# Kernel tuning notes

Hardware: AMD Instinct MI355X
Metric: run time of the kernel (lower is better)

The kernel has to match this reference:

```python
import jax, jax.numpy as jnp
import numpy as np

B, P, ENC = 64, 196, 2048          # batch, num_pixels (14x14), encoder_dim
A, E, D, V = 512, 512, 512, 20000  # attention_dim, embed_dim, decoder_dim, vocab
MAXLEN = 22
T = MAXLEN - 1                     # decode steps (teacher forcing drops last token)


def _lin(k, fan_in, fan_out, scale=0.02):
    return jax.random.normal(k, (fan_in, fan_out), jnp.float32) * scale, jnp.zeros((fan_out,), jnp.float32)


def setup_inputs() -> dict:
    key = jax.random.key(0)
    ks = jax.random.split(key, 16)
    encoder_out = jax.random.normal(ks[0], (B, P, ENC), jnp.float32)
    captions = jax.random.randint(ks[1], (B, MAXLEN), 0, V)
    lens = jax.random.randint(ks[2], (B,), 2, MAXLEN + 1)
    lens = jnp.sort(lens)[::-1].at[0].set(MAXLEN)  # sorted descending, as the torch loop assumes
    emb = jax.random.uniform(ks[3], (V, E), jnp.float32, -0.1, 0.1)
    enc_att_w, enc_att_b = _lin(ks[4], ENC, A)
    dec_att_w, dec_att_b = _lin(ks[5], D, A)
    full_att_w, full_att_b = _lin(ks[6], A, 1)
    w_ih = jax.random.normal(ks[7], (E + ENC, 4 * D), jnp.float32) * 0.02
    w_hh = jax.random.normal(ks[8], (D, 4 * D), jnp.float32) * 0.02
    b_ih = jnp.zeros((4 * D,), jnp.float32)
    b_hh = jnp.zeros((4 * D,), jnp.float32)
    init_h_w, init_h_b = _lin(ks[9], ENC, D)
    init_c_w, init_c_b = _lin(ks[10], ENC, D)
    f_beta_w, f_beta_b = _lin(ks[11], D, ENC)
    fc_w = jax.random.uniform(ks[12], (D, V), jnp.float32, -0.1, 0.1)
    fc_b = jnp.zeros((V,), jnp.float32)
    return dict(encoder_out=encoder_out, captions=captions, lengths=lens, emb=emb,
                enc_att_w=enc_att_w, enc_att_b=enc_att_b, dec_att_w=dec_att_w, dec_att_b=dec_att_b,
                full_att_w=full_att_w, full_att_b=full_att_b, w_ih=w_ih, b_ih=b_ih, w_hh=w_hh, b_hh=b_hh,
                init_h_w=init_h_w, init_h_b=init_h_b, init_c_w=init_c_w, init_c_b=init_c_b,
                f_beta_w=f_beta_w, f_beta_b=f_beta_b, fc_w=fc_w, fc_b=fc_b)


def reference(encoder_out, captions, lengths, emb,
              enc_att_w, enc_att_b, dec_att_w, dec_att_b, full_att_w, full_att_b,
              w_ih, b_ih, w_hh, b_hh, init_h_w, init_h_b, init_c_w, init_c_b,
              f_beta_w, f_beta_b, fc_w, fc_b):
    # Dropout is identity (eval mode) for a deterministic reference.
    dec_len = lengths - 1                       # decode_lengths
    x_emb = emb[captions]                       # (B, L, E)
    mean_enc = encoder_out.mean(axis=1)         # (B, ENC)
    h0 = mean_enc @ init_h_w + init_h_b         # (B, D)
    c0 = mean_enc @ init_c_w + init_c_b
    att1 = encoder_out @ enc_att_w + enc_att_b  # (B, P, A), hoisted out of the loop

    emb_ts = jnp.swapaxes(x_emb[:, :T, :], 0, 1)  # (T, B, E)
    t_idx = jnp.arange(T)

    def step(carry, xt):
        h, c = carry
        e_t, t = xt
        active = (t < dec_len)[:, None]         # ragged batch -> mask (sorted lengths)
        # Bahdanau attention
        att2 = h @ dec_att_w + dec_att_b        # (B, A)
        scores = (jax.nn.relu(att1 + att2[:, None, :]) @ full_att_w)[..., 0] + full_att_b[0]  # (B, P)
        alpha = jax.nn.softmax(scores, axis=1)
        context = jnp.einsum('bp,bpe->be', alpha, encoder_out)
        # gated context
        gate = jax.nn.sigmoid(h @ f_beta_w + f_beta_b)
        context = gate * context
        # LSTMCell (torch gate order i, f, g, o)
        x = jnp.concatenate([e_t, context], axis=1)
        gates = x @ w_ih + h @ w_hh + b_ih + b_hh
        i_g, f_g, g_g, o_g = jnp.split(gates, 4, axis=1)
        c_new = jax.nn.sigmoid(f_g) * c + jax.nn.sigmoid(i_g) * jnp.tanh(g_g)
        h_new = jax.nn.sigmoid(o_g) * jnp.tanh(c_new)
        h = jnp.where(active, h_new, h)
        c = jnp.where(active, c_new, c)
        preds = jnp.where(active, h_new @ fc_w + fc_b, 0.0)
        alpha_o = jnp.where(active, alpha, 0.0)
        return (h, c), (preds, alpha_o)

    _, (preds, alphas) = jax.lax.scan(step, (h0, c0), (emb_ts, t_idx))
    predictions = jnp.swapaxes(preds, 0, 1)     # (B, T, V)
    alphas = jnp.swapaxes(alphas, 0, 1)         # (B, T, P)
    return predictions, alphas
```

## Files before the change

### kernel.cpp

```cpp
#include <hip/hip_runtime.h>

#define BB   64
#define PP   196
#define ENC  2048
#define AA   512
#define EE   512
#define DD   512
#define VV   20000
#define TT   21
#define ML   22

#define PRED_ELEMS ((size_t)BB * TT * VV)

typedef __attribute__((ext_vector_type(8))) short s8bf;
typedef __attribute__((ext_vector_type(4))) float f4acc;

__device__ __forceinline__ float bf2f(unsigned short u) {
    union { unsigned int i; float f; } v; v.i = ((unsigned int)u) << 16; return v.f;
}
__device__ __forceinline__ void unpack2(unsigned int u, float& lo, float& hi) {
    union { unsigned int i; float f; } a, b;
    a.i = u << 16; b.i = u & 0xFFFF0000u; lo = a.f; hi = b.f;
}
__device__ __forceinline__ unsigned short f2bf(float f) {
    union { float f; unsigned int i; } v; v.f = f;
    unsigned int i = v.i;
    return (unsigned short)((i + 0x7FFFu + ((i >> 16) & 1u)) >> 16);
}
__device__ __forceinline__ float sigmoidf(float x) { return 1.0f / (1.0f + __expf(-x)); }

template <bool F> __device__ __forceinline__ float ldw(const void* p, size_t i) {
    if (F) return ((const float*)p)[i];
    return bf2f(((const unsigned short*)p)[i]);
}
template <bool F> __device__ __forceinline__ unsigned short ldbf(const void* p, size_t i) {
    if (F) return f2bf(((const float*)p)[i]);
    return ((const unsigned short*)p)[i];
}
template <bool F> __device__ __forceinline__ float2 ld2(const void* p, size_t i) {
    if (F) return *(const float2*)((const float*)p + i);
    unsigned int u = *(const unsigned int*)((const unsigned short*)p + i);
    float lo, hi; unpack2(u, lo, hi); return make_float2(lo, hi);
}
template <bool F> __device__ __forceinline__ float4 ld4(const void* p, size_t i) {
    if (F) return *(const float4*)((const float*)p + i);
    uint2 u = *(const uint2*)((const unsigned short*)p + i);
    float a, b, c, d; unpack2(u.x, a, b); unpack2(u.y, c, d);
    return make_float4(a, b, c, d);
}
template <bool F> __device__ __forceinline__ void st1(void* p, size_t i, float v) {
    if (F) ((float*)p)[i] = v; else ((unsigned short*)p)[i] = f2bf(v);
}

__global__ void dec_detect_kernel(const unsigned short* __restrict__ enc_us, int* __restrict__ flag) {
    __shared__ int s_cnt;
    if (threadIdx.x == 0) s_cnt = 0;
    __syncthreads();
    int cnt = 0;
    for (int i = threadIdx.x; i < 8192; i += 256) {
        unsigned short u = enc_us[2 * i];
        if ((u & 0x7F80) == 0x7F80) cnt++;
    }
    if (cnt) atomicAdd(&s_cnt, cnt);
    __syncthreads();
    if (threadIdx.x == 0) *flag = (s_cnt > 0) ? 1 : 0;
}

template <bool F>
__device__ __forceinline__ void conv_swz_body(const void* W, int K, int Norig,
                                              unsigned short* dst, int permMode, int nChunks) {
    int chunk = blockIdx.x * 4 + (threadIdx.x >> 6);
    if (chunk >= nChunks) return;
    int lane = threadIdx.x & 63;
    int KC = K >> 5;
    int nt = chunk / KC, kc = chunk % KC;
    int quad = lane >> 4, l15 = lane & 15;
    int np = nt * 16 + l15;
    int col;
    if (permMode == 1) col = ((np >> 4) & 3) * 512 + (np >> 6) * 16 + (np & 15);
    else col = np;
    union { s8bf v; unsigned short s[8]; } o;
    if (np < Norig || permMode == 1) {
        size_t base = (size_t)(kc * 32 + quad * 8) * Norig + col;
#pragma unroll
        for (int j = 0; j < 8; ++j) o.s[j] = ldbf<F>(W, base + (size_t)j * Norig);
    } else {
#pragma unroll
        for (int j = 0; j < 8; ++j) o.s[j] = 0;
    }
    *(s8bf*)(dst + ((size_t)chunk * 64 + lane) * 8) = o.v;
}
__global__ void conv_swz_kernel(const int* __restrict__ flg, const void* __restrict__ W,
                                int K, int Norig, unsigned short* __restrict__ dst,
                                int permMode, int nChunks) {
    if (*flg) conv_swz_body<true>(W, K, Norig, dst, permMode, nChunks);
    else      conv_swz_body<false>(W, K, Norig, dst, permMode, nChunks);
}

template <bool F>
__device__ __forceinline__ void conv_bias_body(const void* dab, const void* fbb,
                                               const void* bih, const void* bhh, const void* fcb,
                                               const void* ihb, const void* icb, const void* eab,
                                               float* ag_b, float* g_b, float* fc_b,
                                               float* ihb_f, float* icb_f, float* eab_f) {
    int i = blockIdx.x * 256 + threadIdx.x;
    if (i < 2560) ag_b[i] = (i < 512) ? ldw<F>(dab, i) : ldw<F>(fbb, i - 512);
    else if (i < 2560 + 2048) {
        int np = i - 2560;
        int orig = ((np >> 4) & 3) * 512 + (np >> 6) * 16 + (np & 15);
        g_b[np] = ldw<F>(bih, orig) + ldw<F>(bhh, orig);
    } else if (i < 2560 + 2048 + 20000) fc_b[i - 4608] = ldw<F>(fcb, i - 4608);
    else if (i < 2560 + 2048 + 20000 + 512) ihb_f[i - 24608] = ldw<F>(ihb, i - 24608);
    else if (i < 2560 + 2048 + 20000 + 1024) icb_f[i - 25120] = ldw<F>(icb, i - 25120);
    else if (i < 2560 + 2048 + 20000 + 1536) eab_f[i - 25632] = ldw<F>(eab, i - 25632);
}
__global__ void conv_bias_kernel(const int* __restrict__ flg,
                                 const void* dab, const void* fbb, const void* bih, const void* bhh,
                                 const void* fcb, const void* ihb, const void* icb, const void* eab,
                                 float* ag_b, float* g_b, float* fc_b,
                                 float* ihb_f, float* icb_f, float* eab_f) {
    if (*flg) conv_bias_body<true>(dab, fbb, bih, bhh, fcb, ihb, icb, eab, ag_b, g_b, fc_b, ihb_f, icb_f, eab_f);
    else      conv_bias_body<false>(dab, fbb, bih, bhh, fcb, ihb, icb, eab, ag_b, g_b, fc_b, ihb_f, icb_f, eab_f);
}

template <bool F>
__device__ __forceinline__ void mean_body(const void* enc, unsigned short* mean_bf) {
    int b = blockIdx.x;
    int e = blockIdx.y * 256 + threadIdx.x;
    size_t base = (size_t)b * PP * ENC + e;
    float s = 0.f;
#pragma unroll 4
    for (int p = 0; p < PP; ++p) s += ldw<F>(enc, base + (size_t)p * ENC);
    mean_bf[b * ENC + e] = f2bf(s * (1.0f / (float)PP));
}
__global__ void dec_mean_kernel(const void* __restrict__ enc, const int* __restrict__ flg,
                                unsigned short* __restrict__ mean_bf) {
    if (*flg) mean_body<true>(enc, mean_bf); else mean_body<false>(enc, mean_bf);
}

__global__ __launch_bounds__(256)
void gemm_u_kernel(const int* __restrict__ flg,
                   const unsigned short* __restrict__ A1, int K1, const unsigned short* __restrict__ W1,
                   const unsigned short* __restrict__ A2, int K2, const unsigned short* __restrict__ W2,
                   const float* __restrict__ bias, int N, int epi, int nct,
                   float* __restrict__ outF, float* __restrict__ outF2,
                   unsigned short* __restrict__ hb, float* __restrict__ cptr,
                   unsigned short* __restrict__ h_all,
                   void* __restrict__ outV, const int* __restrict__ lengths, int t) {
    __shared__ float s_g[4 * 64 * 17];
    int tid = threadIdx.x;
    int wave = tid >> 6, lane = tid & 63;
    int l15 = lane & 15, quad = lane >> 4;
    const unsigned short* Abase1 = A1;
    if (epi == 2) Abase1 = A1 + (size_t)blockIdx.x * 64 * K1;
    f4acc acc[4][2];
#pragma unroll
    for (int a = 0; a < 4; ++a) { acc[a][0] = (f4acc)0.f; acc[a][1] = (f4acc)0.f; }
#pragma unroll
    for (int pass = 0; pass < 2; ++pass) {
        const unsigned short* A = pass ? A2 : Abase1;
        if (!A) continue;
        int K = pass ? K2 : K1;
        const unsigned short* W = pass ? W2 : W1;
        int KC = K >> 5;
        for (int kc = 0; kc < KC; ++kc) {
            s8bf af[4];
#pragma unroll
            for (int rt = 0; rt < 4; ++rt)
                af[rt] = *(const s8bf*)(A + (size_t)(rt * 16 + l15) * K + kc * 32 + quad * 8);
#pragma unroll
            for (int ct = 0; ct < 2; ++ct) if (ct < nct) {
                int nt = blockIdx.y * 4 * nct + ct * 4 + wave;
                s8bf bv = *(const s8bf*)(W + ((size_t)(nt * KC + kc) * 64 + lane) * 8);
#pragma unroll
                for (int rt = 0; rt < 4; ++rt)
                    acc[rt][ct] = __builtin_amdgcn_mfma_f32_16x16x32_bf16(af[rt], bv, acc[rt][ct], 0, 0, 0);
            }
        }
    }
    if (epi == 4) {
        int nl = wave * 16 + l15;
        int g = (nl >> 4) & 3, dl = nl & 15;
        float bv = bias[blockIdx.y * 64 + nl];
#pragma unroll
        for (int rt = 0; rt < 4; ++rt)
#pragma unroll
            for (int r = 0; r < 4; ++r) {
                int m = rt * 16 + quad * 4 + r;
                s_g[(g * 64 + m) * 17 + dl] = acc[rt][0][r] + bv;
            }
        __syncthreads();
        int m = tid >> 2;
        bool act = t < (lengths[m] - 1);
#pragma unroll
        for (int i = 0; i < 4; ++i) {
            int dl2 = (tid & 3) * 4 + i;
            int d = blockIdx.y * 16 + dl2;
            unsigned short hv;
            if (act) {
                float ig = sigmoidf(s_g[(0 * 64 + m) * 17 + dl2]);
                float fg = sigmoidf(s_g[(1 * 64 + m) * 17 + dl2]);
                float gg = tanhf(s_g[(2 * 64 + m) * 17 + dl2]);
                float og = sigmoidf(s_g[(3 * 64 + m) * 17 + dl2]);
                float cn = fg * cptr[m * DD + d] + ig * gg;
                float hn = og * tanhf(cn);
                cptr[m * DD + d] = cn;
                hv = f2bf(hn);
            } else {
                hv = A2[(size_t)m * K2 + d];
            }
            hb[m * DD + d] = hv;
            h_all[((size_t)t * BB + m) * DD + d] = hv;
        }
        return;
    }
    bool f32o = (epi == 2) ? (*flg != 0) : false;
    int tb = blockIdx.x;
#pragma unroll
    for (int ct = 0; ct < 2; ++ct) if (ct < nct) {
        int n = blockIdx.y * 64 * nct + ct * 64 + wave * 16 + l15;
        if (n >= N) continue;
        float bv = bias ? bias[n] : 0.f;
#pragma unroll
        for (int rt = 0; rt < 4; ++rt)
#pragma unroll
            for (int r = 0; r < 4; ++r) {
                int m = rt * 16 + quad * 4 + r;
                float v = acc[rt][ct][r] + bv;
                if (epi == 0)      outF[(size_t)m * N + n] = v;
                else if (epi == 1) {
                    if (n < 512) outF[(size_t)m * 512 + n] = v;
                    else         outF2[(size_t)m * 2048 + (n - 512)] = sigmoidf(v);
                } else if (epi == 3) hb[(size_t)m * DD + n] = f2bf(v);
                else {
                    bool act = tb < (lengths[m] - 1);
                    float pv = act ? v : 0.f;
                    size_t oi = ((size_t)m * TT + tb) * VV + n;
                    if (f32o) ((float*)outV)[oi] = pv; else ((unsigned short*)outV)[oi] = f2bf(pv);
                }
            }
    }
}

template <bool F>
__device__ __forceinline__ void att1_gemm_body(const void* enc, const unsigned short* Wsw,
                                               const float* bias, float* att1) {
    __shared__ __attribute__((aligned(16))) unsigned short As[64 * 40];
    int tid = threadIdx.x;
    int wave = tid >> 6, lane = tid & 63;
    int l15 = lane & 15, quad = lane >> 4;
    int row0 = blockIdx.x * 64;
    f4acc acc[4][2];
#pragma unroll
    for (int a = 0; a < 4; ++a) { acc[a][0] = (f4acc)0.f; acc[a][1] = (f4acc)0.f; }
    int lr = tid >> 2, lk = (tid & 3) * 8;
    for (int kc = 0; kc < 64; ++kc) {
        int k0 = kc * 32;
        if (F) {
            const float* src = (const float*)enc + (size_t)(row0 + lr) * ENC + k0 + lk;
            float4 v0 = *(const float4*)src, v1 = *(const float4*)(src + 4);
            union { s8bf v; unsigned short s[8]; } t8;
            t8.s[0]=f2bf(v0.x); t8.s[1]=f2bf(v0.y); t8.s[2]=f2bf(v0.z); t8.s[3]=f2bf(v0.w);
            t8.s[4]=f2bf(v1.x); t8.s[5]=f2bf(v1.y); t8.s[6]=f2bf(v1.z); t8.s[7]=f2bf(v1.w);
            *(s8bf*)&As[lr * 40 + lk] = t8.v;
        } else {
            *(s8bf*)&As[lr * 40 + lk] =
                *(const s8bf*)((const unsigned short*)enc + (size_t)(row0 + lr) * ENC + k0 + lk);
        }
        __syncthreads();
        s8bf af[4];
#pragma unroll
        for (int rt = 0; rt < 4; ++rt)
            af[rt] = *(const s8bf*)&As[(rt * 16 + l15) * 40 + quad * 8];
#pragma unroll
        for (int ct = 0; ct < 2; ++ct) {
            int nt = blockIdx.y * 8 + ct * 4 + wave;
            s8bf bv = *(const s8bf*)(Wsw + ((size_t)(nt * 64 + kc) * 64 + lane) * 8);
#pragma unroll
            for (int rt = 0; rt < 4; ++rt)
                acc[rt][ct] = __builtin_amdgcn_mfma_f32_16x16x32_bf16(af[rt], bv, acc[rt][ct], 0, 0, 0);
        }
        __syncthreads();
    }
#pragma unroll
    for (int ct = 0; ct < 2; ++ct) {
        int n = blockIdx.y * 128 + ct * 64 + wave * 16 + l15;
        float bv = bias[n];
#pragma unroll
        for (int rt = 0; rt < 4; ++rt)
#pragma unroll
            for (int r = 0; r < 4; ++r) {
                int m = row0 + rt * 16 + quad * 4 + r;
                att1[(size_t)m * AA + n] = acc[rt][ct][r] + bv;
            }
    }
}
__global__ __launch_bounds__(256)
void gemm_att1_kernel(const void* __restrict__ enc, const int* __restrict__ flg,
                      const unsigned short* __restrict__ Wsw, const float* __restrict__ bias,
                      float* __restrict__ att1) {
    if (*flg) att1_gemm_body<true>(enc, Wsw, bias, att1);
    else      att1_gemm_body<false>(enc, Wsw, bias, att1);
}

template <bool F>
__device__ __forceinline__ void att_body(const float* att1, const float* att2,
                                         const void* faw, const void* fab,
                                         const int* lengths, float* alpha_ws, void* out, int t) {
    __shared__ float s_sc[256];
    __shared__ float s_red[256];
    int b = blockIdx.x, tid = threadIdx.x;
    int wave = tid >> 6, lane = tid & 63;
    int a0i = lane * 8;
    float4 a2a = *(const float4*)(att2 + (size_t)b * AA + a0i);
    float4 a2b = *(const float4*)(att2 + (size_t)b * AA + a0i + 4);
    float4 w0 = ld4<F>(faw, a0i);
    float4 w1 = ld4<F>(faw, a0i + 4);
    float fabv = ldw<F>(fab, 0);
    s_sc[tid] = -1e30f;
    __syncthreads();
#pragma unroll 2
    for (int r = wave; r < PP; r += 4) {
        const float4* row = (const float4*)(att1 + ((size_t)b * PP + r) * AA);
        float4 v0 = row[lane * 2];
        float4 v1 = row[lane * 2 + 1];
        float acc = fmaxf(v0.x + a2a.x, 0.f) * w0.x
                  + fmaxf(v0.y + a2a.y, 0.f) * w0.y
                  + fmaxf(v0.z + a2a.z, 0.f) * w0.z
                  + fmaxf(v0.w + a2a.w, 0.f) * w0.w
                  + fmaxf(v1.x + a2b.x, 0.f) * w1.x
                  + fmaxf(v1.y + a2b.y, 0.f) * w1.y
                  + fmaxf(v1.z + a2b.z, 0.f) * w1.z
                  + fmaxf(v1.w + a2b.w, 0.f) * w1.w;
#pragma unroll
        for (int off = 32; off; off >>= 1) acc += __shfl_xor(acc, off, 64);
        if (lane == 0) s_sc[r] = acc + fabv;
    }
    __syncthreads();
    float sc = s_sc[tid];
    s_red[tid] = sc;
    __syncthreads();
    for (int s = 128; s > 0; s >>= 1) { if (tid < s) s_red[tid] = fmaxf(s_red[tid], s_red[tid + s]); __syncthreads(); }
    float m = s_red[0];
    __syncthreads();
    float e = 0.f;
    if (tid < PP) e = __expf(sc - m);
    s_red[tid] = e;
    __syncthreads();
    for (int s = 128; s > 0; s >>= 1) { if (tid < s) s_red[tid] += s_red[tid + s]; __syncthreads(); }
    float inv = 1.0f / s_red[0];
    if (tid < PP) {
        float al = e * inv;
        alpha_ws[b * PP + tid] = al;
        bool active = t < (lengths[b] - 1);
        st1<F>(out, PRED_ELEMS + (size_t)(b * TT + t) * PP + tid, active ? al : 0.f);
    }
}
__global__ void dec_att_kernel(const float* __restrict__ att1, const float* __restrict__ att2,
                               const int* __restrict__ flg,
                               const void* __restrict__ faw, const void* __restrict__ fab,
                               const int* __restrict__ lengths,
                               float* __restrict__ alpha_ws, void* __restrict__ out, int t) {
    if (*flg) att_body<true>(att1, att2, faw, fab, lengths, alpha_ws, out, t);
    else      att_body<false>(att1, att2, faw, fab, lengths, alpha_ws, out, t);
}

template <bool F>
__device__ __forceinline__ void ctx_body(const void* enc, const float* alpha_ws, const float* gate,
                                         const void* emb, const int* captions,
                                         unsigned short* x_bf, int t) {
    __shared__ float s_al[PP];
    int b = blockIdx.x, yc = blockIdx.y, tid = threadIdx.x;
    if (tid < PP) s_al[tid] = alpha_ws[b * PP + tid];
    __syncthreads();
    if (yc == 0) {
        int cap = captions[b * ML + t];
        int i = tid * 2;
        float2 ev = ld2<F>(emb, (size_t)cap * EE + i);
        *(unsigned int*)(x_bf + (size_t)b * 2560 + i) =
            (unsigned int)f2bf(ev.x) | ((unsigned int)f2bf(ev.y) << 16);
    }
    int e = yc * 512 + tid * 2;
    float a0 = 0.f, a1 = 0.f;
    size_t base = (size_t)b * PP * ENC + e;
#pragma unroll 4
    for (int p = 0; p < PP; ++p) {
        float al = s_al[p];
        float2 v = ld2<F>(enc, base + (size_t)p * ENC);
        a0 += al * v.x; a1 += al * v.y;
    }
    float2 g = *(const float2*)&gate[(size_t)b * ENC + e];
    *(unsigned int*)(x_bf + (size_t)b * 2560 + EE + e) =
        (unsigned int)f2bf(a0 * g.x) | ((unsigned int)f2bf(a1 * g.y) << 16);
}
__global__ void dec_ctx_kernel(const void* __restrict__ enc, const int* __restrict__ flg,
                               const float* __restrict__ alpha_ws, const float* __restrict__ gate,
                               const void* __restrict__ emb, const int* __restrict__ captions,
                               unsigned short* __restrict__ x_bf, int t) {
    if (*flg) ctx_body<true>(enc, alpha_ws, gate, emb, captions, x_bf, t);
    else      ctx_body<false>(enc, alpha_ws, gate, emb, captions, x_bf, t);
}

extern "C" void kernel_launch(void* const* d_in, const int* in_sizes, int n_in,
                              void* d_out, int out_size, void* d_ws, size_t ws_size,
                              hipStream_t stream) {
    const void* enc      = d_in[0];
    const int* captions  = (const int*)d_in[1];
    const int* lengths   = (const int*)d_in[2];
    const void* emb      = d_in[3];
    const void* eaw      = d_in[4];
    const void* eab      = d_in[5];
    const void* daw      = d_in[6];
    const void* dab      = d_in[7];
    const void* faw      = d_in[8];
    const void* fab      = d_in[9];
    const void* wih      = d_in[10];
    const void* bih      = d_in[11];
    const void* whh      = d_in[12];
    const void* bhh      = d_in[13];
    const void* ihw      = d_in[14];
    const void* ihb      = d_in[15];
    const void* icw      = d_in[16];
    const void* icb      = d_in[17];
    const void* fbw      = d_in[18];
    const void* fbb      = d_in[19];
    const void* fcw      = d_in[20];
    const void* fcb      = d_in[21];

    char* cur = (char*)d_ws;
    auto alloc = [&](size_t bytes) { void* p = cur; cur += (bytes + 255) & ~(size_t)255; return p; };
    int* flg               = (int*)alloc(4);
    unsigned short* h_bufA = (unsigned short*)alloc((size_t)BB * DD * 2);
    unsigned short* h_bufB = (unsigned short*)alloc((size_t)BB * DD * 2);
    unsigned short* h_all  = (unsigned short*)alloc((size_t)TT * BB * DD * 2);
    unsigned short* x_bf   = (unsigned short*)alloc((size_t)BB * 2560 * 2);
    unsigned short* mean_bf= (unsigned short*)alloc((size_t)BB * ENC * 2);
    float* c               = (float*)alloc((size_t)BB * DD * 4);
    float* att2            = (float*)alloc((size_t)BB * AA * 4);
    float* gate            = (float*)alloc((size_t)BB * ENC * 4);
    float* alpha           = (float*)alloc((size_t)BB * PP * 4);
    float* ag_bias         = (float*)alloc(2560 * 4);
    float* g_bias          = (float*)alloc(2048 * 4);
    float* fc_bias         = (float*)alloc(20000 * 4);
    float* ihb_f           = (float*)alloc(512 * 4);
    float* icb_f           = (float*)alloc(512 * 4);
    float* eab_f           = (float*)alloc(512 * 4);
    unsigned short* eaw_sw = (unsigned short*)alloc((size_t)32 * 64 * 512 * 2);
    unsigned short* ag_sw  = (unsigned short*)alloc((size_t)160 * 16 * 512 * 2);
    unsigned short* ihw_sw = (unsigned short*)alloc((size_t)32 * 64 * 512 * 2);
    unsigned short* icw_sw = (unsigned short*)alloc((size_t)32 * 64 * 512 * 2);
    unsigned short* wih_sw = (unsigned short*)alloc((size_t)128 * 80 * 512 * 2);
    unsigned short* whh_sw = (unsigned short*)alloc((size_t)128 * 16 * 512 * 2);
    unsigned short* fcw_sw = (unsigned short*)alloc((size_t)1256 * 16 * 512 * 2);
    float* att1            = (float*)alloc((size_t)BB * PP * AA * 4);

    dec_detect_kernel<<<1, 256, 0, stream>>>((const unsigned short*)enc, flg);
    conv_swz_kernel<<<(32 * 64 + 3) / 4, 256, 0, stream>>>(flg, eaw, ENC, AA, eaw_sw, 0, 32 * 64);
    conv_swz_kernel<<<(32 * 16 + 3) / 4, 256, 0, stream>>>(flg, daw, DD, AA, ag_sw, 0, 32 * 16);
    conv_swz_kernel<<<(128 * 16 + 3) / 4, 256, 0, stream>>>(flg, fbw, DD, ENC, ag_sw + (size_t)32 * 16 * 512, 0, 128 * 16);
    conv_swz_kernel<<<(32 * 64 + 3) / 4, 256, 0, stream>>>(flg, ihw, ENC, DD, ihw_sw, 0, 32 * 64);
    conv_swz_kernel<<<(32 * 64 + 3) / 4, 256, 0, stream>>>(flg, icw, ENC, DD, icw_sw, 0, 32 * 64);
    conv_swz_kernel<<<(128 * 80 + 3) / 4, 256, 0, stream>>>(flg, wih, 2560, 2048, wih_sw, 1, 128 * 80);
    conv_swz_kernel<<<(128 * 16 + 3) / 4, 256, 0, stream>>>(flg, whh, DD, 2048, whh_sw, 1, 128 * 16);
    conv_swz_kernel<<<(1256 * 16 + 3) / 4, 256, 0, stream>>>(flg, fcw, DD, VV, fcw_sw, 0, 1256 * 16);
    conv_bias_kernel<<<(26144 + 255) / 256, 256, 0, stream>>>(flg, dab, fbb, bih, bhh, fcb, ihb, icb, eab,
                                                              ag_bias, g_bias, fc_bias, ihb_f, icb_f, eab_f);
    dec_mean_kernel<<<dim3(BB, ENC / 256), 256, 0, stream>>>(enc, flg, mean_bf);
    gemm_u_kernel<<<dim3(1, 4), 256, 0, stream>>>(flg, mean_bf, ENC, ihw_sw, nullptr, 0, nullptr,
                                                  ihb_f, DD, 3, 2, nullptr, nullptr, h_bufA, nullptr,
                                                  nullptr, nullptr, nullptr, 0);
    gemm_u_kernel<<<dim3(1, 4), 256, 0, stream>>>(flg, mean_bf, ENC, icw_sw, nullptr, 0, nullptr,
                                                  icb_f, DD, 0, 2, c, nullptr, nullptr, nullptr,
                                                  nullptr, nullptr, nullptr, 0);
    gemm_att1_kernel<<<dim3(196, 4), 256, 0, stream>>>(enc, flg, eaw_sw, eab_f, att1);

    unsigned short* hcur = h_bufA;
    for (int t = 0; t < TT; ++t) {
        unsigned short* hnext = (hcur == h_bufA) ? h_bufB : h_bufA;
        gemm_u_kernel<<<dim3(1, 40), 256, 0, stream>>>(flg, hcur, DD, ag_sw, nullptr, 0, nullptr,
                                                       ag_bias, 2560, 1, 1, att2, gate, nullptr, nullptr,
                                                       nullptr, nullptr, nullptr, 0);
        dec_att_kernel<<<BB, 256, 0, stream>>>(att1, att2, flg, faw, fab, lengths, alpha, d_out, t);
        dec_ctx_kernel<<<dim3(BB, 4), 256, 0, stream>>>(enc, flg, alpha, gate, emb, captions, x_bf, t);
        gemm_u_kernel<<<dim3(1, 32), 256, 0, stream>>>(flg, x_bf, 2560, wih_sw, hcur, DD, whh_sw,
                                                       g_bias, 2048, 4, 1, nullptr, nullptr, hnext, c,
                                                       h_all, nullptr, lengths, t);
        hcur = hnext;
    }
    gemm_u_kernel<<<dim3(TT, 157), 256, 0, stream>>>(flg, h_all, DD, fcw_sw, nullptr, 0, nullptr,
                                                     fc_bias, VV, 2, 2, nullptr, nullptr, nullptr, nullptr,
                                                     nullptr, d_out, lengths, 0);
}
```

Measured before the change: 3.098 ms.

## Store att1 and encoder copy in bf16, widen attention blocks, stage FC output through LDS

att1 is now stored as bf16 instead of fp32, and the attention kernel runs 1024 threads per batch row so each of its 16 waves scores a subset of pixels. When workspace allows, a one-time kernel converts encoder_out to bf16 so the per-step context reduction reads half the bytes. The final vocabulary GEMM epilogue now goes through shared memory and writes vectorized float4/packed bf16 rows instead of strided scalar stores. This halves per-step memory traffic on att1 and the encoder but adds bf16 rounding error to attention scores and context, plus one extra conversion pass and more workspace.

```diff
diff --git a/kernel.cpp b/kernel.cpp
--- a/kernel.cpp
+++ b/kernel.cpp
@@ -64,6 +64,25 @@
     if (cnt) atomicAdd(&s_cnt, cnt);
     __syncthreads();
     if (threadIdx.x == 0) *flag = (s_cnt > 0) ? 1 : 0;
+}
+
+template <bool F>
+__device__ __forceinline__ void encconv_body(const void* enc, unsigned short* dst) {
+    size_t i = ((size_t)blockIdx.x * 256 + threadIdx.x) * 8;
+    if (F) {
+        const float* s = (const float*)enc + i;
+        float4 v0 = *(const float4*)s, v1 = *(const float4*)(s + 4);
+        union { uint4 u; unsigned short h[8]; } o;
+        o.h[0]=f2bf(v0.x); o.h[1]=f2bf(v0.y); o.h[2]=f2bf(v0.z); o.h[3]=f2bf(v0.w);
+        o.h[4]=f2bf(v1.x); o.h[5]=f2bf(v1.y); o.h[6]=f2bf(v1.z); o.h[7]=f2bf(v1.w);
+        *(uint4*)(dst + i) = o.u;
+    } else {
+        *(uint4*)(dst + i) = *(const uint4*)((const unsigned short*)enc + i);
+    }
+}
+__global__ void enc_bf_kernel(const void* __restrict__ enc, const int* __restrict__ flg,
+                              unsigned short* __restrict__ dst) {
+    if (*flg) encconv_body<true>(enc, dst); else encconv_body<false>(enc, dst);
 }
 
 template <bool F>
@@ -147,7 +166,7 @@
                    unsigned short* __restrict__ hb, float* __restrict__ cptr,
                    unsigned short* __restrict__ h_all,
                    void* __restrict__ outV, const int* __restrict__ lengths, int t) {
-    __shared__ float s_g[4 * 64 * 17];
+    __shared__ float s_g[64 * 132];
     int tid = threadIdx.x;
     int wave = tid >> 6, lane = tid & 63;
     int l15 = lane & 15, quad = lane >> 4;
@@ -214,8 +233,46 @@
         }
         return;
     }
-    bool f32o = (epi == 2) ? (*flg != 0) : false;
-    int tb = blockIdx.x;
+    if (epi == 2) {
+        int t2 = blockIdx.x;
+        int base_n = blockIdx.y * 128;
+#pragma unroll
+        for (int ct = 0; ct < 2; ++ct) {
+            int nl = ct * 64 + wave * 16 + l15;
+            int nn = base_n + nl;
+            float bv = (nn < VV) ? bias[nn] : 0.f;
+#pragma unroll
+            for (int rt = 0; rt < 4; ++rt)
+#pragma unroll
+                for (int r = 0; r < 4; ++r) {
+                    int m = rt * 16 + quad * 4 + r;
+                    s_g[m * 132 + nl] = acc[rt][ct][r] + bv;
+                }
+        }
+        __syncthreads();
+        bool f32o = (*flg != 0);
+#pragma unroll
+        for (int pass = 0; pass < 8; ++pass) {
+            int m = pass * 8 + (tid >> 5);
+            int j = tid & 31;
+            int n = base_n + j * 4;
+            if (n < VV) {
+                bool act = t2 < (lengths[m] - 1);
+                float4 v = *(const float4*)&s_g[m * 132 + j * 4];
+                if (!act) { v.x = 0.f; v.y = 0.f; v.z = 0.f; v.w = 0.f; }
+                size_t oi = ((size_t)m * TT + t2) * VV + n;
+                if (f32o) {
+                    *(float4*)((float*)outV + oi) = v;
+                } else {
+                    uint2 pk;
+                    pk.x = (unsigned int)f2bf(v.x) | ((unsigned int)f2bf(v.y) << 16);
+                    pk.y = (unsigned int)f2bf(v.z) | ((unsigned int)f2bf(v.w) << 16);
+                    *(uint2*)((unsigned short*)outV + oi) = pk;
+                }
+            }
+        }
+        return;
+    }
 #pragma unroll
     for (int ct = 0; ct < 2; ++ct) if (ct < nct) {
         int n = blockIdx.y * 64 * nct + ct * 64 + wave * 16 + l15;
@@ -232,19 +289,13 @@
                     if (n < 512) outF[(size_t)m * 512 + n] = v;
                     else         outF2[(size_t)m * 2048 + (n - 512)] = sigmoidf(v);
                 } else if (epi == 3) hb[(size_t)m * DD + n] = f2bf(v);
-                else {
-                    bool act = tb < (lengths[m] - 1);
-                    float pv = act ? v : 0.f;
-                    size_t oi = ((size_t)m * TT + tb) * VV + n;
-                    if (f32o) ((float*)outV)[oi] = pv; else ((unsigned short*)outV)[oi] = f2bf(pv);
-                }
             }
     }
 }
 
 template <bool F>
 __device__ __forceinline__ void att1_gemm_body(const void* enc, const unsigned short* Wsw,
-                                               const float* bias, float* att1) {
+                                               const float* bias, unsigned short* att1) {
     __shared__ __attribute__((aligned(16))) unsigned short As[64 * 40];
     int tid = threadIdx.x;
     int wave = tid >> 6, lane = tid & 63;
@@ -291,20 +342,20 @@
 #pragma unroll
             for (int r = 0; r < 4; ++r) {
                 int m = row0 + rt * 16 + quad * 4 + r;
-                att1[(size_t)m * AA + n] = acc[rt][ct][r] + bv;
+                att1[(size_t)m * AA + n] = f2bf(acc[rt][ct][r] + bv);
             }
     }
 }
 __global__ __launch_bounds__(256)
 void gemm_att1_kernel(const void* __restrict__ enc, const int* __restrict__ flg,
                       const unsigned short* __restrict__ Wsw, const float* __restrict__ bias,
-                      float* __restrict__ att1) {
+                      unsigned short* __restrict__ att1) {
     if (*flg) att1_gemm_body<true>(enc, Wsw, bias, att1);
     else      att1_gemm_body<false>(enc, Wsw, bias, att1);
 }
 
 template <bool F>
-__device__ __forceinline__ void att_body(const float* att1, const float* att2,
+__device__ __forceinline__ void att_body(const unsigned short* att1, const float* att2,
                                          const void* faw, const void* fab,
                                          const int* lengths, float* alpha_ws, void* out, int t) {
     __shared__ float s_sc[256];
@@ -317,35 +368,35 @@
     float4 w0 = ld4<F>(faw, a0i);
     float4 w1 = ld4<F>(faw, a0i + 4);
     float fabv = ldw<F>(fab, 0);
-    s_sc[tid] = -1e30f;
-    __syncthreads();
-#pragma unroll 2
-    for (int r = wave; r < PP; r += 4) {
-        const float4* row = (const float4*)(att1 + ((size_t)b * PP + r) * AA);
-        float4 v0 = row[lane * 2];
-        float4 v1 = row[lane * 2 + 1];
-        float acc = fmaxf(v0.x + a2a.x, 0.f) * w0.x
-                  + fmaxf(v0.y + a2a.y, 0.f) * w0.y
-                  + fmaxf(v0.z + a2a.z, 0.f) * w0.z
-                  + fmaxf(v0.w + a2a.w, 0.f) * w0.w
-                  + fmaxf(v1.x + a2b.x, 0.f) * w1.x
-                  + fmaxf(v1.y + a2b.y, 0.f) * w1.y
-                  + fmaxf(v1.z + a2b.z, 0.f) * w1.z
-                  + fmaxf(v1.w + a2b.w, 0.f) * w1.w;
+    if (tid < 256) s_sc[tid] = -1e30f;
+    __syncthreads();
+    for (int r = wave; r < PP; r += 16) {
+        uint4 u = *(const uint4*)(att1 + ((size_t)b * PP + r) * AA + a0i);
+        float v0, v1, v2, v3, v4, v5, v6, v7;
+        unpack2(u.x, v0, v1); unpack2(u.y, v2, v3);
+        unpack2(u.z, v4, v5); unpack2(u.w, v6, v7);
+        float acc = fmaxf(v0 + a2a.x, 0.f) * w0.x
+                  + fmaxf(v1 + a2a.y, 0.f) * w0.y
+                  + fmaxf(v2 + a2a.z, 0.f) * w0.z
+                  + fmaxf(v3 + a2a.w, 0.f) * w0.w
+                  + fmaxf(v4 + a2b.x, 0.f) * w1.x
+                  + fmaxf(v5 + a2b.y, 0.f) * w1.y
+                  + fmaxf(v6 + a2b.z, 0.f) * w1.z
+                  + fmaxf(v7 + a2b.w, 0.f) * w1.w;
 #pragma unroll
         for (int off = 32; off; off >>= 1) acc += __shfl_xor(acc, off, 64);
         if (lane == 0) s_sc[r] = acc + fabv;
     }
     __syncthreads();
-    float sc = s_sc[tid];
-    s_red[tid] = sc;
+    float sc = (tid < 256) ? s_sc[tid] : -1e30f;
+    if (tid < 256) s_red[tid] = sc;
     __syncthreads();
     for (int s = 128; s > 0; s >>= 1) { if (tid < s) s_red[tid] = fmaxf(s_red[tid], s_red[tid + s]); __syncthreads(); }
     float m = s_red[0];
     __syncthreads();
     float e = 0.f;
     if (tid < PP) e = __expf(sc - m);
-    s_red[tid] = e;
+    if (tid < 256) s_red[tid] = e;
     __syncthreads();
     for (int s = 128; s > 0; s >>= 1) { if (tid < s) s_red[tid] += s_red[tid + s]; __syncthreads(); }
     float inv = 1.0f / s_red[0];
@@ -356,18 +407,19 @@
         st1<F>(out, PRED_ELEMS + (size_t)(b * TT + t) * PP + tid, active ? al : 0.f);
     }
 }
-__global__ void dec_att_kernel(const float* __restrict__ att1, const float* __restrict__ att2,
-                               const int* __restrict__ flg,
-                               const void* __restrict__ faw, const void* __restrict__ fab,
-                               const int* __restrict__ lengths,
-                               float* __restrict__ alpha_ws, void* __restrict__ out, int t) {
+__global__ __launch_bounds__(1024)
+void dec_att_kernel(const unsigned short* __restrict__ att1, const float* __restrict__ att2,
+                    const int* __restrict__ flg,
+                    const void* __restrict__ faw, const void* __restrict__ fab,
+                    const int* __restrict__ lengths,
+                    float* __restrict__ alpha_ws, void* __restrict__ out, int t) {
     if (*flg) att_body<true>(att1, att2, faw, fab, lengths, alpha_ws, out, t);
     else      att_body<false>(att1, att2, faw, fab, lengths, alpha_ws, out, t);
 }
 
 template <bool F>
-__device__ __forceinline__ void ctx_body(const void* enc, const float* alpha_ws, const float* gate,
-                                         const void* emb, const int* captions,
+__device__ __forceinline__ void ctx_body(const void* encp, const float* alpha_ws,
+                                         const float* gate, const void* emb, const int* captions,
                                          unsigned short* x_bf, int t) {
     __shared__ float s_al[PP];
     int b = blockIdx.x, yc = blockIdx.y, tid = threadIdx.x;
@@ -386,19 +438,56 @@
 #pragma unroll 4
     for (int p = 0; p < PP; ++p) {
         float al = s_al[p];
-        float2 v = ld2<F>(enc, base + (size_t)p * ENC);
+        float2 v = ld2<F>(encp, base + (size_t)p * ENC);
         a0 += al * v.x; a1 += al * v.y;
     }
     float2 g = *(const float2*)&gate[(size_t)b * ENC + e];
     *(unsigned int*)(x_bf + (size_t)b * 2560 + EE + e) =
         (unsigned int)f2bf(a0 * g.x) | ((unsigned int)f2bf(a1 * g.y) << 16);
 }
-__global__ void dec_ctx_kernel(const void* __restrict__ enc, const int* __restrict__ flg,
+template <bool FEMB>
+__device__ __forceinline__ void ctx_sel(const void* encp, int forceBf, const float* alpha_ws,
+                                        const float* gate, const void* emb, const int* captions,
+                                        unsigned short* x_bf, int t);
+__global__ void dec_ctx_kernel(const void* __restrict__ encp, const int* __restrict__ flg, int forceBf,
                                const float* __restrict__ alpha_ws, const float* __restrict__ gate,
                                const void* __restrict__ emb, const int* __restrict__ captions,
                                unsigned short* __restrict__ x_bf, int t) {
-    if (*flg) ctx_body<true>(enc, alpha_ws, gate, emb, captions, x_bf, t);
-    else      ctx_body<false>(enc, alpha_ws, gate, emb, captions, x_bf, t);
+    __shared__ float s_al[PP];
+    int b = blockIdx.x, yc = blockIdx.y, tid = threadIdx.x;
+    if (tid < PP) s_al[tid] = alpha_ws[b * PP + tid];
+    __syncthreads();
+    bool f32in = (*flg != 0);
+    if (yc == 0) {
+        int cap = captions[b * ML + t];
+        int i = tid * 2;
+        float2 ev = f32in ? ld2<true>(emb, (size_t)cap * EE + i) : ld2<false>(emb, (size_t)cap * EE + i);
+        *(unsigned int*)(x_bf + (size_t)b * 2560 + i) =
+            (unsigned int)f2bf(ev.x) | ((unsigned int)f2bf(ev.y) << 16);
+    }
+    int e = yc * 512 + tid * 2;
+    float a0 = 0.f, a1 = 0.f;
+    size_t base = (size_t)b * PP * ENC + e;
+    bool encF32 = f32in && !forceBf;
+    if (encF32) {
+#pragma unroll 4
+        for (int p = 0; p < PP; ++p) {
+            float al = s_al[p];
+            float2 v = *(const float2*)((const float*)encp + base + (size_t)p * ENC);
+            a0 += al * v.x; a1 += al * v.y;
+        }
+    } else {
+#pragma unroll 4
+        for (int p = 0; p < PP; ++p) {
+            float al = s_al[p];
+            unsigned int u = *(const unsigned int*)((const unsigned short*)encp + base + (size_t)p * ENC);
+            float lo, hi; unpack2(u, lo, hi);
+            a0 += al * lo; a1 += al * hi;
+        }
+    }
+    float2 g = *(const float2*)&gate[(size_t)b * ENC + e];
+    *(unsigned int*)(x_bf + (size_t)b * 2560 + EE + e) =
+        (unsigned int)f2bf(a0 * g.x) | ((unsigned int)f2bf(a1 * g.y) << 16);
 }
 
 extern "C" void kernel_launch(void* const* d_in, const int* in_sizes, int n_in,
@@ -452,9 +541,15 @@
     unsigned short* wih_sw = (unsigned short*)alloc((size_t)128 * 80 * 512 * 2);
     unsigned short* whh_sw = (unsigned short*)alloc((size_t)128 * 16 * 512 * 2);
     unsigned short* fcw_sw = (unsigned short*)alloc((size_t)1256 * 16 * 512 * 2);
-    float* att1            = (float*)alloc((size_t)BB * PP * AA * 4);
+    unsigned short* att1_bf= (unsigned short*)alloc((size_t)BB * PP * AA * 2);
+    size_t enc_bf_bytes = (size_t)BB * PP * ENC * 2;
+    size_t used = (size_t)(cur - (char*)d_ws);
+    bool have_enc_bf = (used + enc_bf_bytes + 256 <= ws_size);
+    unsigned short* enc_bf = have_enc_bf ? (unsigned short*)alloc(enc_bf_bytes) : nullptr;
 
     dec_detect_kernel<<<1, 256, 0, stream>>>((const unsigned short*)enc, flg);
+    if (have_enc_bf)
+        enc_bf_kernel<<<(BB * PP * ENC) / (256 * 8), 256, 0, stream>>>(enc, flg, enc_bf);
     conv_swz_kernel<<<(32 * 64 + 3) / 4, 256, 0, stream>>>(flg, eaw, ENC, AA, eaw_sw, 0, 32 * 64);
     conv_swz_kernel<<<(32 * 16 + 3) / 4, 256, 0, stream>>>(flg, daw, DD, AA, ag_sw, 0, 32 * 16);
     conv_swz_kernel<<<(128 * 16 + 3) / 4, 256, 0, stream>>>(flg, fbw, DD, ENC, ag_sw + (size_t)32 * 16 * 512, 0, 128 * 16);
@@ -472,16 +567,18 @@
     gemm_u_kernel<<<dim3(1, 4), 256, 0, stream>>>(flg, mean_bf, ENC, icw_sw, nullptr, 0, nullptr,
                                                   icb_f, DD, 0, 2, c, nullptr, nullptr, nullptr,
                                                   nullptr, nullptr, nullptr, 0);
-    gemm_att1_kernel<<<dim3(196, 4), 256, 0, stream>>>(enc, flg, eaw_sw, eab_f, att1);
-
+    gemm_att1_kernel<<<dim3(196, 4), 256, 0, stream>>>(enc, flg, eaw_sw, eab_f, att1_bf);
+
+    const void* ctx_enc = have_enc_bf ? (const void*)enc_bf : enc;
+    int forceBf = have_enc_bf ? 1 : 0;
     unsigned short* hcur = h_bufA;
     for (int t = 0; t < TT; ++t) {
         unsigned short* hnext = (hcur == h_bufA) ? h_bufB : h_bufA;
         gemm_u_kernel<<<dim3(1, 40), 256, 0, stream>>>(flg, hcur, DD, ag_sw, nullptr, 0, nullptr,
                                                        ag_bias, 2560, 1, 1, att2, gate, nullptr, nullptr,
                                                        nullptr, nullptr, nullptr, 0);
-        dec_att_kernel<<<BB, 256, 0, stream>>>(att1, att2, flg, faw, fab, lengths, alpha, d_out, t);
-        dec_ctx_kernel<<<dim3(BB, 4), 256, 0, stream>>>(enc, flg, alpha, gate, emb, captions, x_bf, t);
+        dec_att_kernel<<<BB, 1024, 0, stream>>>(att1_bf, att2, flg, faw, fab, lengths, alpha, d_out, t);
+        dec_ctx_kernel<<<dim3(BB, 4), 256, 0, stream>>>(ctx_enc, flg, forceBf, alpha, gate, emb, captions, x_bf, t);
         gemm_u_kernel<<<dim3(1, 32), 256, 0, stream>>>(flg, x_bf, 2560, wih_sw, hcur, DD, whh_sw,
                                                        g_bias, 2048, 4, 1, nullptr, nullptr, hnext, c,
                                                        h_all, nullptr, lengths, t);
```

Result: faster. 2.754 ms (-11.1%).
